# Kernel tuning notes

Hardware: AMD Instinct MI355X
Metric: run time of the kernel (lower is better)

## Reference

```python
import jax, jax.numpy as jnp
import numpy as np

B, N, D, L = 32, 1024, 128, 2  # batch graphs, nodes, hidden dim, num GIN layers
BN_EPS = 1e-5


def _batchnorm(x2d, gamma, beta):
    # Training-mode BatchNorm1d over flattened (B*N, D) with biased variance
    mean = jnp.mean(x2d, axis=0)
    var = jnp.mean(jnp.square(x2d - mean), axis=0)
    return (x2d - mean) * (gamma / jnp.sqrt(var + BN_EPS)) + beta


def setup_inputs() -> dict:
    key = jax.random.key(0)
    ks = jax.random.split(key, 12)
    s = 1.0 / np.sqrt(D)  # torch Linear default init scale
    inp = {
        "x": jax.random.normal(ks[0], (B, N, D), dtype=jnp.float32),
        "padded_nei": jax.random.randint(ks[1], (B, N, 8), 0, N, dtype=jnp.int64),
        "adj": jax.random.uniform(ks[2], (B, N, N), dtype=jnp.float32),
        # stacked per-layer params [L, ...]
        "W1": jax.random.uniform(ks[3], (L, D, D), jnp.float32, -s, s),
        "b1": jax.random.uniform(ks[4], (L, D), jnp.float32, -s, s),
        "W2": jax.random.uniform(ks[5], (L, D, D), jnp.float32, -s, s),
        "b2": jax.random.uniform(ks[6], (L, D), jnp.float32, -s, s),
        "g_in": jnp.ones((L, D), jnp.float32),   # MLP-internal BN gamma
        "be_in": jnp.zeros((L, D), jnp.float32),  # MLP-internal BN beta
        "g_out": jnp.ones((L, D), jnp.float32),  # GraphCNN outer BN gamma
        "be_out": jnp.zeros((L, D), jnp.float32),
    }
    return inp


def reference(x, padded_nei, adj, W1, b1, W2, b2, g_in, be_in, g_out, be_out):
    h = x  # [B, N, D]
    for l in range(L):
        # sum-pooling over neighbors via batched dense adjacency matmul
        pooled = jnp.einsum('bij,bjd->bid', adj, h)  # [B, N, D]
        # MLP: Linear -> BN -> ReLU -> Linear
        z = pooled @ W1[l] + b1[l]
        z = jax.nn.relu(_batchnorm(z.reshape(-1, D), g_in[l], be_in[l])).reshape(B, N, D)
        z = z @ W2[l] + b2[l]
        # outer BatchNorm1d + ReLU
        h = jax.nn.relu(_batchnorm(z.reshape(-1, D), g_out[l], be_out[l])).reshape(B, N, D)
    return h
```

## Files before the change

### kernel.cpp

```cpp
#include <hip/hip_runtime.h>
#include <stdint.h>


#define BB 32
#define NN 1024
#define DD 128
#define RR 32768

typedef __bf16 bf16_t;
typedef bf16_t bf16x8 __attribute__((ext_vector_type(8)));
typedef float f32x4 __attribute__((ext_vector_type(4)));

__device__ __forceinline__ unsigned short f2b(float f) {
  unsigned u = __float_as_uint(f);
  u += 0x7fff + ((u >> 16) & 1);
  return (unsigned short)(u >> 16);
}

__global__ __launch_bounds__(256) void k0_xT(const float* __restrict__ x,
                                             unsigned short* __restrict__ hT) {
  const int b = blockIdx.x, nt = blockIdx.y, tid = threadIdx.x;
  __shared__ alignas(16) unsigned short T[128][136];
  const int r = tid >> 1, c0 = (tid & 1) * 64;
  const float* src = x + ((size_t)(b * 8 + nt) * 128 + r) * 128 + c0;
#pragma unroll
  for (int i = 0; i < 64; i += 4) {
    float4 v = *(const float4*)(src + i);
    int c = c0 + i;
    T[c][r] = f2b(v.x); T[c + 1][r] = f2b(v.y);
    T[c + 2][r] = f2b(v.z); T[c + 3][r] = f2b(v.w);
  }
  __syncthreads();
  const int d = tid >> 1, n0 = (tid & 1) * 64;
  unsigned short* dst = hT + ((size_t)b * DD + d) * NN + nt * 128 + n0;
#pragma unroll
  for (int i = 0; i < 64; i += 8)
    *(uint4*)(dst + i) = *(const uint4*)&T[d][n0 + i];
}

__global__ __launch_bounds__(256) void k0_wT(const float* __restrict__ W1,
                                             const float* __restrict__ W2,
                                             unsigned short* __restrict__ W1T,
                                             unsigned short* __restrict__ W2T) {
  int idx = blockIdx.x * 256 + threadIdx.x;
  int w = idx >> 15;
  int rem = idx & 32767;
  int l = rem >> 14;
  int n = (rem >> 7) & 127;
  int k = rem & 127;
  const float* W = w ? W2 : W1;
  unsigned short* WT = w ? W2T : W1T;
  WT[((size_t)l * 128 + n) * 128 + k] = f2b(W[((size_t)l * 128 + k) * 128 + n]);
}

__global__ __launch_bounds__(256) void k1_pool(const float* __restrict__ adj,
                                               const unsigned short* __restrict__ hT,
                                               unsigned short* __restrict__ pooled) {
  const int mt = blockIdx.x, b = blockIdx.y;
  const int tid = threadIdx.x;
  const int wave = tid >> 6, lane = tid & 63;
  const int wr = (wave >> 1) * 64, wc = (wave & 1) * 64;
  const int ln = lane & 15, q = lane >> 4;

  __shared__ alignas(16) unsigned short As[128][40];
  __shared__ alignas(16) unsigned short Bs[128][40];

  const float* adjb = adj + ((size_t)b * NN + mt * 128) * NN;
  const unsigned short* hTb = hT + (size_t)b * DD * NN;

  f32x4 acc[4][4];
  f32x4 zero = {0.f, 0.f, 0.f, 0.f};
#pragma unroll
  for (int i = 0; i < 4; i++)
#pragma unroll
    for (int j = 0; j < 4; j++) acc[i][j] = zero;

  const int rs = tid >> 1;
  const int hs = tid & 1;

  for (int k0 = 0; k0 < NN; k0 += 32) {
    __syncthreads();
    {
      const float* src = adjb + (size_t)rs * NN + k0 + hs * 16;
      alignas(16) unsigned short t[16];
#pragma unroll
      for (int i = 0; i < 16; i += 4) {
        float4 v = *(const float4*)(src + i);
        t[i] = f2b(v.x); t[i + 1] = f2b(v.y); t[i + 2] = f2b(v.z); t[i + 3] = f2b(v.w);
      }
      *(uint4*)&As[rs][hs * 16] = *(const uint4*)&t[0];
      *(uint4*)&As[rs][hs * 16 + 8] = *(const uint4*)&t[8];
    }
    {
      const unsigned short* src = hTb + (size_t)rs * NN + k0 + hs * 16;
      *(uint4*)&Bs[rs][hs * 16] = *(const uint4*)(src);
      *(uint4*)&Bs[rs][hs * 16 + 8] = *(const uint4*)(src + 8);
    }
    __syncthreads();
    bf16x8 af[4], bfr[4];
#pragma unroll
    for (int i = 0; i < 4; i++) af[i] = *(const bf16x8*)&As[wr + i * 16 + ln][q * 8];
#pragma unroll
    for (int j = 0; j < 4; j++) bfr[j] = *(const bf16x8*)&Bs[wc + j * 16 + ln][q * 8];
#pragma unroll
    for (int i = 0; i < 4; i++)
#pragma unroll
      for (int j = 0; j < 4; j++)
        acc[i][j] = __builtin_amdgcn_mfma_f32_16x16x32_bf16(af[i], bfr[j], acc[i][j], 0, 0, 0);
  }

  unsigned short* outb = pooled + ((size_t)b * NN + mt * 128) * DD;
#pragma unroll
  for (int i = 0; i < 4; i++) {
    int row = wr + i * 16 + q * 4;
#pragma unroll
    for (int j = 0; j < 4; j++) {
      int col = wc + j * 16 + ln;
#pragma unroll
      for (int r = 0; r < 4; r++)
        outb[(size_t)(row + r) * DD + col] = f2b(acc[i][j][r]);
    }
  }
}

__global__ __launch_bounds__(256) void k2_lin(const unsigned short* __restrict__ Ain,
                                              const unsigned short* __restrict__ WT,
                                              const float* __restrict__ bias,
                                              float* __restrict__ Z,
                                              float* __restrict__ gsum,
                                              float* __restrict__ gsq) {
  const int mt = blockIdx.x;
  const int tid = threadIdx.x;
  const int wave = tid >> 6, lane = tid & 63;
  const int wr = (wave >> 1) * 64, wc = (wave & 1) * 64;
  const int ln = lane & 15, q = lane >> 4;

  __shared__ alignas(16) unsigned short As[128][40];
  __shared__ alignas(16) unsigned short Ws[128][136];
  __shared__ float lsum[128], lsq[128];

  if (tid < 128) { lsum[tid] = 0.f; lsq[tid] = 0.f; }
#pragma unroll
  for (int p = 0; p < 8; p++) {
    int c = tid + p * 256;
    int n = c >> 4, k8 = (c & 15) * 8;
    *(uint4*)&Ws[n][k8] = *(const uint4*)&WT[n * 128 + k8];
  }

  f32x4 acc[4][4];
  f32x4 zero = {0.f, 0.f, 0.f, 0.f};
#pragma unroll
  for (int i = 0; i < 4; i++)
#pragma unroll
    for (int j = 0; j < 4; j++) acc[i][j] = zero;

  const int rs = tid >> 1, hs = tid & 1;
  const size_t row0 = (size_t)mt * 128;

  for (int k0 = 0; k0 < 128; k0 += 32) {
    __syncthreads();
    const unsigned short* src = Ain + (row0 + rs) * 128 + k0 + hs * 16;
    *(uint4*)&As[rs][hs * 16] = *(const uint4*)src;
    *(uint4*)&As[rs][hs * 16 + 8] = *(const uint4*)(src + 8);
    __syncthreads();
    bf16x8 af[4], bfr[4];
#pragma unroll
    for (int i = 0; i < 4; i++) af[i] = *(const bf16x8*)&As[wr + i * 16 + ln][q * 8];
#pragma unroll
    for (int j = 0; j < 4; j++) bfr[j] = *(const bf16x8*)&Ws[wc + j * 16 + ln][k0 + q * 8];
#pragma unroll
    for (int i = 0; i < 4; i++)
#pragma unroll
      for (int j = 0; j < 4; j++)
        acc[i][j] = __builtin_amdgcn_mfma_f32_16x16x32_bf16(af[i], bfr[j], acc[i][j], 0, 0, 0);
  }

  float s1[4] = {0.f, 0.f, 0.f, 0.f}, s2[4] = {0.f, 0.f, 0.f, 0.f};
  float* Zb = Z + row0 * 128;
#pragma unroll
  for (int j = 0; j < 4; j++) {
    int col = wc + j * 16 + ln;
    float bc = bias[col];
#pragma unroll
    for (int i = 0; i < 4; i++) {
      int row = wr + i * 16 + q * 4;
#pragma unroll
      for (int r = 0; r < 4; r++) {
        float v = acc[i][j][r] + bc;
        Zb[(size_t)(row + r) * 128 + col] = v;
        s1[j] += v; s2[j] += v * v;
      }
    }
  }
#pragma unroll
  for (int j = 0; j < 4; j++) {
    s1[j] += __shfl_xor(s1[j], 16); s1[j] += __shfl_xor(s1[j], 32);
    s2[j] += __shfl_xor(s2[j], 16); s2[j] += __shfl_xor(s2[j], 32);
  }
  if (q == 0) {
#pragma unroll
    for (int j = 0; j < 4; j++) {
      atomicAdd(&lsum[wc + j * 16 + ln], s1[j]);
      atomicAdd(&lsq[wc + j * 16 + ln], s2[j]);
    }
  }
  __syncthreads();
  if (tid < 128) atomicAdd(&gsum[tid], lsum[tid]);
  else atomicAdd(&gsq[tid - 128], lsq[tid - 128]);
}

__global__ __launch_bounds__(256) void k3_lin(const float* __restrict__ Zin,
                                              const float* __restrict__ gsum_in,
                                              const float* __restrict__ gsq_in,
                                              const float* __restrict__ gamma,
                                              const float* __restrict__ beta,
                                              const unsigned short* __restrict__ WT,
                                              const float* __restrict__ bias,
                                              float* __restrict__ Z,
                                              float* __restrict__ gsum,
                                              float* __restrict__ gsq) {
  const int mt = blockIdx.x;
  const int tid = threadIdx.x;
  const int wave = tid >> 6, lane = tid & 63;
  const int wr = (wave >> 1) * 64, wc = (wave & 1) * 64;
  const int ln = lane & 15, q = lane >> 4;

  __shared__ alignas(16) unsigned short As[128][40];
  __shared__ alignas(16) unsigned short Ws[128][136];
  __shared__ float lsum[128], lsq[128];
  __shared__ float nsc[128], nsh[128];

  if (tid < 128) {
    float mean = gsum_in[tid] * (1.f / 32768.f);
    float var = gsq_in[tid] * (1.f / 32768.f) - mean * mean;
    float sc = gamma[tid] * rsqrtf(var + 1e-5f);
    nsc[tid] = sc; nsh[tid] = beta[tid] - mean * sc;
    lsum[tid] = 0.f; lsq[tid] = 0.f;
  }
#pragma unroll
  for (int p = 0; p < 8; p++) {
    int c = tid + p * 256;
    int n = c >> 4, k8 = (c & 15) * 8;
    *(uint4*)&Ws[n][k8] = *(const uint4*)&WT[n * 128 + k8];
  }

  f32x4 acc[4][4];
  f32x4 zero = {0.f, 0.f, 0.f, 0.f};
#pragma unroll
  for (int i = 0; i < 4; i++)
#pragma unroll
    for (int j = 0; j < 4; j++) acc[i][j] = zero;

  const int rs = tid >> 1, hs = tid & 1;
  const size_t row0 = (size_t)mt * 128;

  for (int k0 = 0; k0 < 128; k0 += 32) {
    __syncthreads();
    {
      const float* src = Zin + (row0 + rs) * 128 + k0 + hs * 16;
      alignas(16) unsigned short t[16];
#pragma unroll
      for (int i = 0; i < 16; i += 4) {
        float4 v = *(const float4*)(src + i);
        int c = k0 + hs * 16 + i;
        t[i]     = f2b(fmaxf(fmaf(v.x, nsc[c], nsh[c]), 0.f));
        t[i + 1] = f2b(fmaxf(fmaf(v.y, nsc[c + 1], nsh[c + 1]), 0.f));
        t[i + 2] = f2b(fmaxf(fmaf(v.z, nsc[c + 2], nsh[c + 2]), 0.f));
        t[i + 3] = f2b(fmaxf(fmaf(v.w, nsc[c + 3], nsh[c + 3]), 0.f));
      }
      *(uint4*)&As[rs][hs * 16] = *(const uint4*)&t[0];
      *(uint4*)&As[rs][hs * 16 + 8] = *(const uint4*)&t[8];
    }
    __syncthreads();
    bf16x8 af[4], bfr[4];
#pragma unroll
    for (int i = 0; i < 4; i++) af[i] = *(const bf16x8*)&As[wr + i * 16 + ln][q * 8];
#pragma unroll
    for (int j = 0; j < 4; j++) bfr[j] = *(const bf16x8*)&Ws[wc + j * 16 + ln][k0 + q * 8];
#pragma unroll
    for (int i = 0; i < 4; i++)
#pragma unroll
      for (int j = 0; j < 4; j++)
        acc[i][j] = __builtin_amdgcn_mfma_f32_16x16x32_bf16(af[i], bfr[j], acc[i][j], 0, 0, 0);
  }

  float s1[4] = {0.f, 0.f, 0.f, 0.f}, s2[4] = {0.f, 0.f, 0.f, 0.f};
  float* Zb = Z + row0 * 128;
#pragma unroll
  for (int j = 0; j < 4; j++) {
    int col = wc + j * 16 + ln;
    float bc = bias[col];
#pragma unroll
    for (int i = 0; i < 4; i++) {
      int row = wr + i * 16 + q * 4;
#pragma unroll
      for (int r = 0; r < 4; r++) {
        float v = acc[i][j][r] + bc;
        Zb[(size_t)(row + r) * 128 + col] = v;
        s1[j] += v; s2[j] += v * v;
      }
    }
  }
#pragma unroll
  for (int j = 0; j < 4; j++) {
    s1[j] += __shfl_xor(s1[j], 16); s1[j] += __shfl_xor(s1[j], 32);
    s2[j] += __shfl_xor(s2[j], 16); s2[j] += __shfl_xor(s2[j], 32);
  }
  if (q == 0) {
#pragma unroll
    for (int j = 0; j < 4; j++) {
      atomicAdd(&lsum[wc + j * 16 + ln], s1[j]);
      atomicAdd(&lsq[wc + j * 16 + ln], s2[j]);
    }
  }
  __syncthreads();
  if (tid < 128) atomicAdd(&gsum[tid], lsum[tid]);
  else atomicAdd(&gsq[tid - 128], lsq[tid - 128]);
}

__global__ __launch_bounds__(256) void k4_bnt(const float* __restrict__ Z,
                                              const float* __restrict__ gsum,
                                              const float* __restrict__ gsq,
                                              const float* __restrict__ gamma,
                                              const float* __restrict__ beta,
                                              unsigned short* __restrict__ hT) {
  const int b = blockIdx.x, nt = blockIdx.y, tid = threadIdx.x;
  __shared__ alignas(16) unsigned short T[128][136];
  __shared__ float nsc[128], nsh[128];
  if (tid < 128) {
    float mean = gsum[tid] * (1.f / 32768.f);
    float var = gsq[tid] * (1.f / 32768.f) - mean * mean;
    float sc = gamma[tid] * rsqrtf(var + 1e-5f);
    nsc[tid] = sc; nsh[tid] = beta[tid] - mean * sc;
  }
  __syncthreads();
  const int r = tid >> 1, c0 = (tid & 1) * 64;
  const float* src = Z + ((size_t)(b * 8 + nt) * 128 + r) * 128 + c0;
#pragma unroll
  for (int i = 0; i < 64; i += 4) {
    float4 v = *(const float4*)(src + i);
    int c = c0 + i;
    T[c][r]     = f2b(fmaxf(fmaf(v.x, nsc[c], nsh[c]), 0.f));
    T[c + 1][r] = f2b(fmaxf(fmaf(v.y, nsc[c + 1], nsh[c + 1]), 0.f));
    T[c + 2][r] = f2b(fmaxf(fmaf(v.z, nsc[c + 2], nsh[c + 2]), 0.f));
    T[c + 3][r] = f2b(fmaxf(fmaf(v.w, nsc[c + 3], nsh[c + 3]), 0.f));
  }
  __syncthreads();
  const int d = tid >> 1, n0 = (tid & 1) * 64;
  unsigned short* dst = hT + ((size_t)b * DD + d) * NN + nt * 128 + n0;
#pragma unroll
  for (int i = 0; i < 64; i += 8)
    *(uint4*)(dst + i) = *(const uint4*)&T[d][n0 + i];
}

__global__ __launch_bounds__(256) void k4_out(const float* __restrict__ Z,
                                              const float* __restrict__ gsum,
                                              const float* __restrict__ gsq,
                                              const float* __restrict__ gamma,
                                              const float* __restrict__ beta,
                                              float* __restrict__ out) {
  const int blk = blockIdx.x, tid = threadIdx.x;
  __shared__ float nsc[128], nsh[128];
  if (tid < 128) {
    float mean = gsum[tid] * (1.f / 32768.f);
    float var = gsq[tid] * (1.f / 32768.f) - mean * mean;
    float sc = gamma[tid] * rsqrtf(var + 1e-5f);
    nsc[tid] = sc; nsh[tid] = beta[tid] - mean * sc;
  }
  __syncthreads();
  const int r = tid >> 1, c0 = (tid & 1) * 64;
  const float* src = Z + ((size_t)blk * 128 + r) * 128 + c0;
  float* dst = out + ((size_t)blk * 128 + r) * 128 + c0;
#pragma unroll
  for (int i = 0; i < 64; i += 4) {
    float4 v = *(const float4*)(src + i);
    int c = c0 + i;
    float4 o;
    o.x = fmaxf(fmaf(v.x, nsc[c], nsh[c]), 0.f);
    o.y = fmaxf(fmaf(v.y, nsc[c + 1], nsh[c + 1]), 0.f);
    o.z = fmaxf(fmaf(v.z, nsc[c + 2], nsh[c + 2]), 0.f);
    o.w = fmaxf(fmaf(v.w, nsc[c + 3], nsh[c + 3]), 0.f);
    *(float4*)(dst + i) = o;
  }
}

extern "C" void kernel_launch(void* const* d_in, const int* in_sizes, int n_in,
                              void* d_out, int out_size, void* d_ws, size_t ws_size,
                              hipStream_t stream) {
  const float* x = (const float*)d_in[0];
  const float* adj = (const float*)d_in[2];
  const float* W1 = (const float*)d_in[3];
  const float* b1 = (const float*)d_in[4];
  const float* W2 = (const float*)d_in[5];
  const float* b2 = (const float*)d_in[6];
  const float* g_in = (const float*)d_in[7];
  const float* be_in = (const float*)d_in[8];
  const float* g_out = (const float*)d_in[9];
  const float* be_out = (const float*)d_in[10];
  float* out = (float*)d_out;

  char* ws = (char*)d_ws;
  unsigned short* hT = (unsigned short*)ws;
  float* z1 = (float*)(ws + 8ull * 1024 * 1024);
  float* z2 = (float*)(ws + 24ull * 1024 * 1024);
  unsigned short* pooled = (unsigned short*)(ws + 24ull * 1024 * 1024);
  unsigned short* W1T = (unsigned short*)(ws + 40ull * 1024 * 1024);
  unsigned short* W2T = W1T + 2 * 128 * 128;
  float* stats = (float*)(ws + 40ull * 1024 * 1024 + 256 * 1024);

  hipMemsetAsync(stats, 0, 4 * 256 * sizeof(float), stream);

  k0_xT<<<dim3(32, 8), 256, 0, stream>>>(x, hT);
  k0_wT<<<256, 256, 0, stream>>>(W1, W2, W1T, W2T);

  for (int l = 0; l < 2; l++) {
    float* st_in = stats + (l * 2 + 0) * 256;
    float* st_out = stats + (l * 2 + 1) * 256;
    k1_pool<<<dim3(8, 32), 256, 0, stream>>>(adj, hT, pooled);
    k2_lin<<<256, 256, 0, stream>>>(pooled, W1T + l * 16384, b1 + l * 128, z1,
                                    st_in, st_in + 128);
    k3_lin<<<256, 256, 0, stream>>>(z1, st_in, st_in + 128, g_in + l * 128,
                                    be_in + l * 128, W2T + l * 16384, b2 + l * 128,
                                    z2, st_out, st_out + 128);
    if (l == 0)
      k4_bnt<<<dim3(32, 8), 256, 0, stream>>>(z2, st_out, st_out + 128, g_out,
                                              be_out, hT);
    else
      k4_out<<<256, 256, 0, stream>>>(z2, st_out, st_out + 128, g_out + 128,
                                      be_out + 128, out);
  }
}
```

Measured before the change: 379.0 us.

## Pre-convert adjacency to bf16 once and register-prefetch pooling tiles with K=64

Adds a pre-pass that converts the fp32 adjacency to bf16 once, so both pooling layers read half the bytes and skip per-tile conversion. The pooling kernel now uses 64-wide K tiles and prefetches the next tile into registers while the current one is computed. The trade is an extra full read/write pass over the adjacency (128MB read, 64MB written), more workspace, and higher register and LDS use per block.

```diff
diff --git a/kernel.cpp b/kernel.cpp
--- a/kernel.cpp
+++ b/kernel.cpp
@@ -15,6 +15,20 @@
   unsigned u = __float_as_uint(f);
   u += 0x7fff + ((u >> 16) & 1);
   return (unsigned short)(u >> 16);
+}
+
+__global__ __launch_bounds__(256) void k0_adj(const float* __restrict__ adj,
+                                              unsigned short* __restrict__ adj16) {
+  const size_t i = ((size_t)blockIdx.x * 256 + threadIdx.x) * 16;
+  alignas(16) unsigned short t[16];
+#pragma unroll
+  for (int u = 0; u < 4; u++) {
+    float4 v = *(const float4*)(adj + i + u * 4);
+    t[u * 4] = f2b(v.x); t[u * 4 + 1] = f2b(v.y);
+    t[u * 4 + 2] = f2b(v.z); t[u * 4 + 3] = f2b(v.w);
+  }
+  *(uint4*)(adj16 + i) = *(const uint4*)&t[0];
+  *(uint4*)(adj16 + i + 8) = *(const uint4*)&t[8];
 }
 
 __global__ __launch_bounds__(256) void k0_xT(const float* __restrict__ x,
@@ -53,7 +67,7 @@
   WT[((size_t)l * 128 + n) * 128 + k] = f2b(W[((size_t)l * 128 + k) * 128 + n]);
 }
 
-__global__ __launch_bounds__(256) void k1_pool(const float* __restrict__ adj,
+__global__ __launch_bounds__(256) void k1_pool(const unsigned short* __restrict__ adj16,
                                                const unsigned short* __restrict__ hT,
                                                unsigned short* __restrict__ pooled) {
   const int mt = blockIdx.x, b = blockIdx.y;
@@ -62,10 +76,10 @@
   const int wr = (wave >> 1) * 64, wc = (wave & 1) * 64;
   const int ln = lane & 15, q = lane >> 4;
 
-  __shared__ alignas(16) unsigned short As[128][40];
-  __shared__ alignas(16) unsigned short Bs[128][40];
-
-  const float* adjb = adj + ((size_t)b * NN + mt * 128) * NN;
+  __shared__ alignas(16) unsigned short As[128][72];
+  __shared__ alignas(16) unsigned short Bs[128][72];
+
+  const unsigned short* adjb = adj16 + ((size_t)b * NN + mt * 128) * NN;
   const unsigned short* hTb = hT + (size_t)b * DD * NN;
 
   f32x4 acc[4][4];
@@ -76,37 +90,50 @@
     for (int j = 0; j < 4; j++) acc[i][j] = zero;
 
   const int rs = tid >> 1;
-  const int hs = tid & 1;
-
-  for (int k0 = 0; k0 < NN; k0 += 32) {
-    __syncthreads();
-    {
-      const float* src = adjb + (size_t)rs * NN + k0 + hs * 16;
-      alignas(16) unsigned short t[16];
-#pragma unroll
-      for (int i = 0; i < 16; i += 4) {
-        float4 v = *(const float4*)(src + i);
-        t[i] = f2b(v.x); t[i + 1] = f2b(v.y); t[i + 2] = f2b(v.z); t[i + 3] = f2b(v.w);
+  const int c0 = (tid & 1) * 32;
+
+  const unsigned short* pA = adjb + (size_t)rs * NN + c0;
+  const unsigned short* pB = hTb + (size_t)rs * NN + c0;
+
+  uint4 pa[4], pb[4];
+#pragma unroll
+  for (int u = 0; u < 4; u++) {
+    pa[u] = *(const uint4*)(pA + u * 8);
+    pb[u] = *(const uint4*)(pB + u * 8);
+  }
+
+  for (int k0 = 0; k0 < NN; k0 += 64) {
+    __syncthreads();
+#pragma unroll
+    for (int u = 0; u < 4; u++) {
+      *(uint4*)&As[rs][c0 + u * 8] = pa[u];
+      *(uint4*)&Bs[rs][c0 + u * 8] = pb[u];
+    }
+    __syncthreads();
+    if (k0 + 64 < NN) {
+      const unsigned short* qA = pA + k0 + 64;
+      const unsigned short* qB = pB + k0 + 64;
+#pragma unroll
+      for (int u = 0; u < 4; u++) {
+        pa[u] = *(const uint4*)(qA + u * 8);
+        pb[u] = *(const uint4*)(qB + u * 8);
       }
-      *(uint4*)&As[rs][hs * 16] = *(const uint4*)&t[0];
-      *(uint4*)&As[rs][hs * 16 + 8] = *(const uint4*)&t[8];
-    }
-    {
-      const unsigned short* src = hTb + (size_t)rs * NN + k0 + hs * 16;
-      *(uint4*)&Bs[rs][hs * 16] = *(const uint4*)(src);
-      *(uint4*)&Bs[rs][hs * 16 + 8] = *(const uint4*)(src + 8);
-    }
-    __syncthreads();
-    bf16x8 af[4], bfr[4];
-#pragma unroll
-    for (int i = 0; i < 4; i++) af[i] = *(const bf16x8*)&As[wr + i * 16 + ln][q * 8];
-#pragma unroll
-    for (int j = 0; j < 4; j++) bfr[j] = *(const bf16x8*)&Bs[wc + j * 16 + ln][q * 8];
-#pragma unroll
-    for (int i = 0; i < 4; i++)
+    }
+#pragma unroll
+    for (int kk = 0; kk < 2; kk++) {
+      bf16x8 af[4], bfr[4];
+#pragma unroll
+      for (int i = 0; i < 4; i++)
+        af[i] = *(const bf16x8*)&As[wr + i * 16 + ln][kk * 32 + q * 8];
 #pragma unroll
       for (int j = 0; j < 4; j++)
-        acc[i][j] = __builtin_amdgcn_mfma_f32_16x16x32_bf16(af[i], bfr[j], acc[i][j], 0, 0, 0);
+        bfr[j] = *(const bf16x8*)&Bs[wc + j * 16 + ln][kk * 32 + q * 8];
+#pragma unroll
+      for (int i = 0; i < 4; i++)
+#pragma unroll
+        for (int j = 0; j < 4; j++)
+          acc[i][j] = __builtin_amdgcn_mfma_f32_16x16x32_bf16(af[i], bfr[j], acc[i][j], 0, 0, 0);
+    }
   }
 
   unsigned short* outb = pooled + ((size_t)b * NN + mt * 128) * DD;
@@ -407,16 +434,18 @@
   unsigned short* W1T = (unsigned short*)(ws + 40ull * 1024 * 1024);
   unsigned short* W2T = W1T + 2 * 128 * 128;
   float* stats = (float*)(ws + 40ull * 1024 * 1024 + 256 * 1024);
+  unsigned short* adj16 = (unsigned short*)(ws + 48ull * 1024 * 1024);
 
   hipMemsetAsync(stats, 0, 4 * 256 * sizeof(float), stream);
 
+  k0_adj<<<8192, 256, 0, stream>>>(adj, adj16);
   k0_xT<<<dim3(32, 8), 256, 0, stream>>>(x, hT);
   k0_wT<<<256, 256, 0, stream>>>(W1, W2, W1T, W2T);
 
   for (int l = 0; l < 2; l++) {
     float* st_in = stats + (l * 2 + 0) * 256;
     float* st_out = stats + (l * 2 + 1) * 256;
-    k1_pool<<<dim3(8, 32), 256, 0, stream>>>(adj, hT, pooled);
+    k1_pool<<<dim3(8, 32), 256, 0, stream>>>(adj16, hT, pooled);
     k2_lin<<<256, 256, 0, stream>>>(pooled, W1T + l * 16384, b1 + l * 128, z1,
                                     st_in, st_in + 128);
     k3_lin<<<256, 256, 0, stream>>>(z1, st_in, st_in + 128, g_in + l * 128,
```

New measurement: 435.6 us. 14.9% more time.
